# Kernel optimization log

Measured on AMD Instinct MI355X. Metric: run time of the kernel, lower is better.

## Reference

```python
import jax, jax.numpy as jnp
import numpy as np

N_NODES = 100000
N_EDGES = 1600000
N_GRAPHS = 1000
NODES_PER_GRAPH = 100  # batch vector is arange(N)//100: exactly 100 nodes per graph
HID = 32
MAX_Z = 1000
K = 30
D_LAT = HID * 3 + 1  # 97, total_latent_dim


def setup_inputs() -> dict:
    key = jax.random.key(0)
    ks = jax.random.split(key, 24)
    s = 1.0 / np.sqrt(HID)
    inp = {
        "z": jax.random.randint(ks[0], (N_NODES,), 0, MAX_Z, dtype=jnp.int32),
        "edge_index": jax.random.randint(ks[1], (2, N_EDGES), 0, N_NODES, dtype=jnp.int32),
        "batch": (jnp.arange(N_NODES, dtype=jnp.int32) // NODES_PER_GRAPH),
        "edge_weight": jax.random.uniform(ks[2], (N_EDGES,), jnp.float32, 0.1, 1.0),
        "z_emb": jax.random.normal(ks[3], (MAX_Z, HID), jnp.float32) * 0.1,
        # GCNConv stack: [32->32, 32->32, 32->32, 32->1]
        "Wg1": jax.random.normal(ks[4], (HID, HID)) * s,
        "bg1": jnp.zeros((HID,), jnp.float32),
        "Wg2": jax.random.normal(ks[5], (HID, HID)) * s,
        "bg2": jnp.zeros((HID,), jnp.float32),
        "Wg3": jax.random.normal(ks[6], (HID, HID)) * s,
        "bg3": jnp.zeros((HID,), jnp.float32),
        "Wg4": jax.random.normal(ks[7], (HID, 1)) * s,
        "bg4": jnp.zeros((1,), jnp.float32),
        # Conv1d(1, 16, kernel=97, stride=97)
        "Wc1": jax.random.normal(ks[8], (16, D_LAT)) * (1.0 / np.sqrt(D_LAT)),
        "bc1": jnp.zeros((16,), jnp.float32),
        # Conv1d(16, 32, kernel=5, stride=1)
        "Wc2": jax.random.normal(ks[9], (32, 16, 5)) * (1.0 / np.sqrt(16 * 5)),
        "bc2": jnp.zeros((32,), jnp.float32),
        # Linear(352, 128), Linear(128, 1)
        "Wl1": jax.random.normal(ks[10], (352, 128)) * (1.0 / np.sqrt(352)),
        "bl1": jnp.zeros((128,), jnp.float32),
        "Wl2": jax.random.normal(ks[11], (128, 1)) * (1.0 / np.sqrt(128)),
        "bl2": jnp.zeros((1,), jnp.float32),
    }
    return inp


def gcn_conv(x, src, dst, ew, W, b, n):
    # PyG GCNConv: xW, add self-loops (weight 1), sym-normalize, aggregate at dst, + bias
    xw = x @ W
    deg = jax.ops.segment_sum(ew, dst, num_segments=n) + 1.0  # +1 for self loop
    dinv = jnp.where(deg > 0, jax.lax.rsqrt(deg), 0.0)
    norm = dinv[src] * ew * dinv[dst]                          # [E]
    out = jax.ops.segment_sum(norm[:, None] * xw[src], dst, num_segments=n)
    out = out + xw * (dinv * dinv)[:, None]                    # self-loop term
    return out + b


def _forward(z, edge_index, batch, edge_weight, z_emb, Wg1, bg1, Wg2, bg2, Wg3, bg3,
             Wg4, bg4, Wc1, bc1, Wc2, bc2, Wl1, bl1, Wl2, bl2):
    src, dst = edge_index[0], edge_index[1]
    n = z.shape[0]
    x = z_emb[z]                                              # [N, 32]
    xs = []
    h = x
    for W, b in ((Wg1, bg1), (Wg2, bg2), (Wg3, bg3), (Wg4, bg4)):
        h = jnp.tanh(gcn_conv(h, src, dst, edge_weight, W, b, n))
        xs.append(h)
    x = jnp.concatenate(xs, axis=-1)                          # [N, 97]
    # global_sort_pool: batch is uniform (100 nodes/graph) so dense batching is a reshape
    dense = x.reshape(N_GRAPHS, NODES_PER_GRAPH, D_LAT)       # [B, 100, 97]
    idx = jnp.argsort(-dense[:, :, -1], axis=1)[:, :K]        # sort desc by last channel
    top = jnp.take_along_axis(dense, idx[:, :, None], axis=1)  # [B, 30, 97]
    # Conv1d(1,16,97,stride=97) on flattened [B,1,30*97] == per-slot dense layer
    y = jax.nn.relu(jnp.einsum('bkd,cd->bck', top, Wc1) + bc1[None, :, None])  # [B,16,30]
    y = y.reshape(N_GRAPHS, 16, K // 2, 2).max(axis=-1)        # MaxPool1d(2,2) -> [B,16,15]
    y = jax.lax.conv_general_dilated(y, Wc2, (1,), 'VALID',
                                     dimension_numbers=('NCH', 'OIH', 'NCH'))
    y = jax.nn.relu(y + bc2[None, :, None])                    # [B,32,11]
    y = y.reshape(N_GRAPHS, -1)                                # [B,352]
    y = jax.nn.relu(y @ Wl1 + bl1)                             # dropout: eval mode, identity
    return y @ Wl2 + bl2                                       # [B,1]


def reference(z, edge_index, batch, edge_weight, z_emb, Wg1, bg1, Wg2, bg2, Wg3, bg3,
              Wg4, bg4, Wc1, bc1, Wc2, bc2, Wl1, bl1, Wl2, bl2):
    return _forward(z, edge_index, batch, edge_weight, z_emb, Wg1, bg1, Wg2, bg2, Wg3,
                    bg3, Wg4, bg4, Wc1, bc1, Wc2, bc2, Wl1, bl1, Wl2, bl2)
```

## Files before the change

kernel.cpp:

```cpp
#include <hip/hip_runtime.h>

#define HID 32
#define DLAT 97
#define NPG 100
#define TOPK 30
#define BKT_NODES 256
#define MAXBKT 512
#define EPB 4096


__global__ void binA_kernel(const int* __restrict__ dst, int* __restrict__ bucket_cnt, int E) {
    __shared__ int hist[MAXBKT];
    for (int t = threadIdx.x; t < MAXBKT; t += blockDim.x) hist[t] = 0;
    __syncthreads();
    int base = blockIdx.x * EPB;
    int lim = min(E, base + EPB);
    for (int e = base + threadIdx.x; e < lim; e += blockDim.x)
        atomicAdd(&hist[dst[e] >> 8], 1);
    __syncthreads();
    for (int t = threadIdx.x; t < MAXBKT; t += blockDim.x) {
        int v = hist[t];
        if (v) atomicAdd(&bucket_cnt[t], v);
    }
}

__global__ __launch_bounds__(MAXBKT) void bscan_kernel(const int* __restrict__ bucket_cnt,
                                                       int* __restrict__ bucket_start,
                                                       int* __restrict__ cursor) {
    __shared__ int sh[MAXBKT];
    int t = threadIdx.x;
    int v = bucket_cnt[t];
    sh[t] = v;
    __syncthreads();
    for (int off = 1; off < MAXBKT; off <<= 1) {
        int tv = (t >= off) ? sh[t - off] : 0;
        __syncthreads();
        sh[t] += tv;
        __syncthreads();
    }
    int excl = sh[t] - v;
    bucket_start[t] = excl;
    cursor[t] = excl;
    if (t == MAXBKT - 1) bucket_start[MAXBKT] = sh[t];
}

__global__ void binB_kernel(const int* __restrict__ src, const int* __restrict__ dst,
                            const float* __restrict__ ew, int* __restrict__ cursor,
                            int2* __restrict__ bedge, int E) {
    __shared__ int hist[MAXBKT];
    __shared__ int lcur[MAXBKT];
    for (int t = threadIdx.x; t < MAXBKT; t += blockDim.x) hist[t] = 0;
    __syncthreads();
    int base = blockIdx.x * EPB;
    int lim = min(E, base + EPB);
    for (int e = base + threadIdx.x; e < lim; e += blockDim.x)
        atomicAdd(&hist[dst[e] >> 8], 1);
    __syncthreads();
    for (int t = threadIdx.x; t < MAXBKT; t += blockDim.x) {
        int v = hist[t];
        lcur[t] = v ? atomicAdd(&cursor[t], v) : 0;
    }
    __syncthreads();
    for (int e = base + threadIdx.x; e < lim; e += blockDim.x) {
        int d = dst[e];
        int slot = atomicAdd(&lcur[d >> 8], 1);
        bedge[slot] = make_int2(src[e] | ((d & 255) << 20), __float_as_int(ew[e]));
    }
}

__global__ __launch_bounds__(BKT_NODES) void sortlocal_kernel(
    const int2* __restrict__ bedge, const int* __restrict__ bucket_start,
    int2* __restrict__ csr, int* __restrict__ row_start, float* __restrict__ dinv,
    int N, int E) {
    __shared__ int cnt[BKT_NODES];
    __shared__ float facc[BKT_NODES];
    __shared__ int sh[BKT_NODES];
    __shared__ int lcur[BKT_NODES];
    int b = blockIdx.x;
    int beg = bucket_start[b], end = bucket_start[b + 1];
    int t = threadIdx.x;
    cnt[t] = 0;
    facc[t] = 0.f;
    __syncthreads();
    for (int i = beg + t; i < end; i += BKT_NODES) {
        int2 e = bedge[i];
        int loc = e.x >> 20;
        atomicAdd(&cnt[loc], 1);
        atomicAdd(&facc[loc], __int_as_float(e.y));
    }
    __syncthreads();
    int n = b * BKT_NODES + t;
    if (n < N) dinv[n] = 1.0f / sqrtf(1.0f + facc[t]);
    int v = cnt[t];
    sh[t] = v;
    __syncthreads();
    for (int off = 1; off < BKT_NODES; off <<= 1) {
        int tv = (t >= off) ? sh[t - off] : 0;
        __syncthreads();
        sh[t] += tv;
        __syncthreads();
    }
    int excl = sh[t] - v;
    lcur[t] = excl;
    if (n < N) row_start[n] = beg + excl;
    if (b == 0 && t == 0) row_start[N] = E;
    __syncthreads();
    for (int i = beg + t; i < end; i += BKT_NODES) {
        int2 e = bedge[i];
        int slot = atomicAdd(&lcur[e.x >> 20], 1);
        csr[beg + slot] = make_int2(e.x & 0xFFFFF, e.y);
    }
}

__global__ void xw1_kernel(const int* __restrict__ z, const float* __restrict__ z_emb,
                           const float* __restrict__ W, const float* __restrict__ dinv,
                           float* __restrict__ xw, int N) {
    int tid = blockIdx.x * blockDim.x + threadIdx.x;
    if (tid >= N * HID) return;
    int n = tid >> 5, f = tid & 31;
    const float* row = z_emb + (size_t)z[n] * HID;
    float s = 0.f;
#pragma unroll
    for (int k = 0; k < HID; ++k) s += row[k] * W[k * HID + f];
    xw[tid] = s * dinv[n];
}

template <int MODE>
__global__ __launch_bounds__(256) void agg32f_kernel(
    const int* __restrict__ row_start, const int2* __restrict__ csr,
    const float* __restrict__ xw, const float* __restrict__ b,
    const float* __restrict__ dinv, const float* __restrict__ Wn,
    float* __restrict__ concat, int col_off, float* __restrict__ xw_next, int N) {
    int tid = blockIdx.x * blockDim.x + threadIdx.x;
    int n = tid >> 5;
    if (n >= N) return;
    int f = threadIdx.x & 31;
    int beg = row_start[n], end = row_start[n + 1];
    float s0 = 0.f, s1 = 0.f;
    for (int i = beg; i < end; i += 8) {
        float w[8];
        int idx[8];
#pragma unroll
        for (int j = 0; j < 8; ++j) {
            int ii = min(i + j, end - 1);
            int2 v = csr[ii];
            idx[j] = v.x;
            w[j] = (i + j < end) ? __int_as_float(v.y) : 0.f;
        }
        float x[8];
#pragma unroll
        for (int j = 0; j < 8; ++j) x[j] = xw[(size_t)idx[j] * HID + f];
#pragma unroll
        for (int j = 0; j < 8; ++j) {
            if (j & 1) s1 += w[j] * x[j];
            else       s0 += w[j] * x[j];
        }
    }
    float s = s0 + s1;
    float di = dinv[n];
    float outv = tanhf(di * (s + xw[(size_t)n * HID + f]) + b[f]);
    concat[(size_t)n * DLAT + col_off + f] = outv;

    if (MODE == 0) {
        float p = 0.f;
#pragma unroll
        for (int k = 0; k < HID; ++k) {
            float ok = __shfl(outv, k, 32);
            p += ok * Wn[k * HID + f];
        }
        xw_next[(size_t)n * HID + f] = p * di;
    } else {
        float p = outv * Wn[f];
        p += __shfl_xor(p, 16);
        p += __shfl_xor(p, 8);
        p += __shfl_xor(p, 4);
        p += __shfl_xor(p, 2);
        p += __shfl_xor(p, 1);
        if (f == 0) xw_next[n] = p * di;
    }
}

__global__ __launch_bounds__(128) void topk_head_kernel(
    const int* __restrict__ row_start, const int2* __restrict__ csr,
    const float* __restrict__ xw4, const float* __restrict__ b4,
    const float* __restrict__ dinv, const float* __restrict__ concat,
    const float* __restrict__ Wc1, const float* __restrict__ bc1,
    const float* __restrict__ Wc2, const float* __restrict__ bc2,
    const float* __restrict__ Wl1, const float* __restrict__ bl1,
    const float* __restrict__ Wl2, const float* __restrict__ bl2,
    float* __restrict__ out) {
    int g = blockIdx.x;
    int tid = threadIdx.x;
    __shared__ float v[NPG];
    __shared__ int tidx[TOPK];
    __shared__ float tval[TOPK];
    __shared__ float top[TOPK * DLAT];
    __shared__ float y1[16 * TOPK];
    __shared__ float y2[16 * 15];
    __shared__ float y3[352];
    __shared__ float r[128];

    if (tid < NPG) {
        int n = g * NPG + tid;
        int beg = row_start[n], end = row_start[n + 1];
        float s = 0.f;
        for (int i = beg; i < end; ++i) {
            int2 e = csr[i];
            s += __int_as_float(e.y) * xw4[e.x];
        }
        v[tid] = tanhf(dinv[n] * (s + xw4[n]) + b4[0]);
    }
    __syncthreads();
    if (tid < NPG) {
        float vi = v[tid];
        int cnt = 0;
#pragma unroll 4
        for (int j = 0; j < NPG; ++j) {
            float vj = v[j];
            cnt += (vj > vi) || (vj == vi && j < tid);
        }
        if (cnt < TOPK) {
            tidx[cnt] = g * NPG + tid;
            tval[cnt] = vi;
        }
    }
    __syncthreads();

    for (int idx = tid; idx < TOPK * DLAT; idx += 128) {
        int k = idx / DLAT, d = idx - k * DLAT;
        top[idx] = (d == 96) ? tval[k] : concat[(size_t)tidx[k] * DLAT + d];
    }
    __syncthreads();

    for (int idx = tid; idx < 16 * TOPK; idx += 128) {
        int c = idx / TOPK, k = idx % TOPK;
        float s = bc1[c];
        const float* w = Wc1 + c * DLAT;
        const float* t = top + k * DLAT;
#pragma unroll 4
        for (int d = 0; d < DLAT; ++d) s += t[d] * w[d];
        y1[c * TOPK + k] = fmaxf(s, 0.f);
    }
    __syncthreads();

    for (int idx = tid; idx < 16 * 15; idx += 128) {
        int c = idx / 15, j = idx % 15;
        y2[idx] = fmaxf(y1[c * TOPK + 2 * j], y1[c * TOPK + 2 * j + 1]);
    }
    __syncthreads();

    for (int idx = tid; idx < 352; idx += 128) {
        int o = idx / 11, t = idx % 11;
        float s = bc2[o];
#pragma unroll
        for (int i = 0; i < 16; ++i) {
#pragma unroll
            for (int k = 0; k < 5; ++k)
                s += Wc2[(o * 16 + i) * 5 + k] * y2[i * 15 + t + k];
        }
        y3[idx] = fmaxf(s, 0.f);
    }
    __syncthreads();

    {
        float s = bl1[tid];
        for (int d = 0; d < 352; ++d) s += y3[d] * Wl1[d * 128 + tid];
        r[tid] = fmaxf(s, 0.f) * Wl2[tid];
    }
    __syncthreads();
    if (tid < 64) r[tid] += r[tid + 64];
    __syncthreads();
    if (tid == 0) {
        float s = 0.f;
        for (int j = 0; j < 64; ++j) s += r[j];
        out[g] = s + bl2[0];
    }
}


extern "C" void kernel_launch(void* const* d_in, const int* in_sizes, int n_in,
                              void* d_out, int out_size, void* d_ws, size_t ws_size,
                              hipStream_t stream) {
    const int* z = (const int*)d_in[0];
    const int* ei = (const int*)d_in[1];
    const float* ew = (const float*)d_in[3];
    const float* z_emb = (const float*)d_in[4];
    const float* Wg[4] = {(const float*)d_in[5], (const float*)d_in[7],
                          (const float*)d_in[9], (const float*)d_in[11]};
    const float* bg[4] = {(const float*)d_in[6], (const float*)d_in[8],
                          (const float*)d_in[10], (const float*)d_in[12]};
    const float* Wc1 = (const float*)d_in[13];
    const float* bc1 = (const float*)d_in[14];
    const float* Wc2 = (const float*)d_in[15];
    const float* bc2 = (const float*)d_in[16];
    const float* Wl1 = (const float*)d_in[17];
    const float* bl1 = (const float*)d_in[18];
    const float* Wl2 = (const float*)d_in[19];
    const float* bl2 = (const float*)d_in[20];
    float* out = (float*)d_out;

    const int N = in_sizes[0];
    const int E = in_sizes[1] / 2;
    const int G = out_size;
    const int* src = ei;
    const int* dst = ei + E;

    auto cdiv = [](long long a, long long b) { return (int)((a + b - 1) / b); };
    const int NB = cdiv(E, EPB);
    const int NBKT = cdiv(N, BKT_NODES);

    char* ws = (char*)d_ws;
    int2* bedge = (int2*)ws;                  ws += sizeof(int2) * (size_t)E;
    int2* csr = (int2*)ws;                    ws += sizeof(int2) * (size_t)E;
    int* bucket_cnt = (int*)ws;               ws += sizeof(int) * MAXBKT;
    int* bucket_start = (int*)ws;             ws += sizeof(int) * (MAXBKT + 1);
    int* cursor = (int*)ws;                   ws += sizeof(int) * MAXBKT;
    int* row_start = (int*)ws;                ws += sizeof(int) * (N + 1);
    float* dinv = (float*)ws;                 ws += sizeof(float) * N;
    float* xw_a = (float*)ws;                 ws += sizeof(float) * (size_t)N * HID;
    float* concat = (float*)ws;               ws += sizeof(float) * (size_t)N * DLAT;
    float* xw4 = (float*)ws;                  ws += sizeof(float) * N;
    float* xw_b = (float*)bedge;

    const int B = 256;

    hipMemsetAsync(bucket_cnt, 0, sizeof(int) * MAXBKT, stream);
    binA_kernel<<<NB, B, 0, stream>>>(dst, bucket_cnt, E);
    bscan_kernel<<<1, MAXBKT, 0, stream>>>(bucket_cnt, bucket_start, cursor);
    binB_kernel<<<NB, B, 0, stream>>>(src, dst, ew, cursor, bedge, E);
    sortlocal_kernel<<<NBKT, BKT_NODES, 0, stream>>>(bedge, bucket_start, csr, row_start,
                                                     dinv, N, E);

    xw1_kernel<<<cdiv((long long)N * HID, B), B, 0, stream>>>(z, z_emb, Wg[0], dinv, xw_a, N);
    const int AGGB = cdiv((long long)N * 32, B);
    agg32f_kernel<0><<<AGGB, B, 0, stream>>>(row_start, csr, xw_a, bg[0], dinv, Wg[1],
                                             concat, 0, xw_b, N);
    agg32f_kernel<0><<<AGGB, B, 0, stream>>>(row_start, csr, xw_b, bg[1], dinv, Wg[2],
                                             concat, 32, xw_a, N);
    agg32f_kernel<1><<<AGGB, B, 0, stream>>>(row_start, csr, xw_a, bg[2], dinv, Wg[3],
                                             concat, 64, xw4, N);

    topk_head_kernel<<<G, 128, 0, stream>>>(row_start, csr, xw4, bg[3], dinv, concat,
                                            Wc1, bc1, Wc2, bc2, Wl1, bl1, Wl2, bl2, out);
}
```

Before: 423.1 us.

## Stage bucket edges in LDS and shrink buckets for CSR build

```diff
diff --git a/kernel.cpp b/kernel.cpp
--- a/kernel.cpp
+++ b/kernel.cpp
@@ -4,21 +4,24 @@
 #define DLAT 97
 #define NPG 100
 #define TOPK 30
-#define BKT_NODES 256
-#define MAXBKT 512
-#define EPB 4096
-
-
-__global__ void binA_kernel(const int* __restrict__ dst, int* __restrict__ bucket_cnt, int E) {
+#define BKT_NODES 128
+#define BKT_SHIFT 7
+#define MAXBKT 1024
+#define CAP 3072
+#define CHUNK 8192
+
+
+__global__ __launch_bounds__(256) void binA_kernel(const int* __restrict__ dst,
+                                                   int* __restrict__ bucket_cnt, int E) {
     __shared__ int hist[MAXBKT];
-    for (int t = threadIdx.x; t < MAXBKT; t += blockDim.x) hist[t] = 0;
-    __syncthreads();
-    int base = blockIdx.x * EPB;
-    int lim = min(E, base + EPB);
-    for (int e = base + threadIdx.x; e < lim; e += blockDim.x)
-        atomicAdd(&hist[dst[e] >> 8], 1);
-    __syncthreads();
-    for (int t = threadIdx.x; t < MAXBKT; t += blockDim.x) {
+    for (int t = threadIdx.x; t < MAXBKT; t += 256) hist[t] = 0;
+    __syncthreads();
+    int base = blockIdx.x * CHUNK;
+    int lim = min(E, base + CHUNK);
+    for (int e = base + threadIdx.x; e < lim; e += 256)
+        atomicAdd(&hist[dst[e] >> BKT_SHIFT], 1);
+    __syncthreads();
+    for (int t = threadIdx.x; t < MAXBKT; t += 256) {
         int v = hist[t];
         if (v) atomicAdd(&bucket_cnt[t], v);
     }
@@ -44,71 +47,119 @@
     if (t == MAXBKT - 1) bucket_start[MAXBKT] = sh[t];
 }
 
-__global__ void binB_kernel(const int* __restrict__ src, const int* __restrict__ dst,
-                            const float* __restrict__ ew, int* __restrict__ cursor,
-                            int2* __restrict__ bedge, int E) {
+__global__ __launch_bounds__(256) void binB_kernel(const int* __restrict__ src,
+                                                   const int* __restrict__ dst,
+                                                   const float* __restrict__ ew,
+                                                   int* __restrict__ cursor,
+                                                   int2* __restrict__ bedge, int E) {
     __shared__ int hist[MAXBKT];
     __shared__ int lcur[MAXBKT];
-    for (int t = threadIdx.x; t < MAXBKT; t += blockDim.x) hist[t] = 0;
-    __syncthreads();
-    int base = blockIdx.x * EPB;
-    int lim = min(E, base + EPB);
-    for (int e = base + threadIdx.x; e < lim; e += blockDim.x)
-        atomicAdd(&hist[dst[e] >> 8], 1);
-    __syncthreads();
-    for (int t = threadIdx.x; t < MAXBKT; t += blockDim.x) {
+    __shared__ int dcache[CHUNK];
+    for (int t = threadIdx.x; t < MAXBKT; t += 256) hist[t] = 0;
+    __syncthreads();
+    int base = blockIdx.x * CHUNK;
+    int M = min(E - base, CHUNK);
+    for (int i = threadIdx.x; i < M; i += 256) {
+        int d = dst[base + i];
+        dcache[i] = d;
+        atomicAdd(&hist[d >> BKT_SHIFT], 1);
+    }
+    __syncthreads();
+    for (int t = threadIdx.x; t < MAXBKT; t += 256) {
         int v = hist[t];
         lcur[t] = v ? atomicAdd(&cursor[t], v) : 0;
     }
     __syncthreads();
-    for (int e = base + threadIdx.x; e < lim; e += blockDim.x) {
-        int d = dst[e];
-        int slot = atomicAdd(&lcur[d >> 8], 1);
-        bedge[slot] = make_int2(src[e] | ((d & 255) << 20), __float_as_int(ew[e]));
-    }
-}
-
-__global__ __launch_bounds__(BKT_NODES) void sortlocal_kernel(
+    for (int i = threadIdx.x; i < M; i += 256) {
+        int d = dcache[i];
+        int slot = atomicAdd(&lcur[d >> BKT_SHIFT], 1);
+        bedge[slot] = make_int2(src[base + i] | ((d & (BKT_NODES - 1)) << 20),
+                                __float_as_int(ew[base + i]));
+    }
+}
+
+__global__ __launch_bounds__(256) void sortlocal_kernel(
     const int2* __restrict__ bedge, const int* __restrict__ bucket_start,
     int2* __restrict__ csr, int* __restrict__ row_start, float* __restrict__ dinv,
     int N, int E) {
+    __shared__ int2 LDSe[CAP];
     __shared__ int cnt[BKT_NODES];
-    __shared__ float facc[BKT_NODES];
     __shared__ int sh[BKT_NODES];
     __shared__ int lcur[BKT_NODES];
-    int b = blockIdx.x;
-    int beg = bucket_start[b], end = bucket_start[b + 1];
-    int t = threadIdx.x;
-    cnt[t] = 0;
-    facc[t] = 0.f;
-    __syncthreads();
-    for (int i = beg + t; i < end; i += BKT_NODES) {
-        int2 e = bedge[i];
-        int loc = e.x >> 20;
-        atomicAdd(&cnt[loc], 1);
-        atomicAdd(&facc[loc], __int_as_float(e.y));
-    }
+    __shared__ float facc[BKT_NODES];
+    int b = blockIdx.x, t = threadIdx.x;
+    int beg = bucket_start[b], end = bucket_start[b + 1], M = end - beg;
+    if (t < BKT_NODES) { cnt[t] = 0; facc[t] = 0.f; }
     __syncthreads();
     int n = b * BKT_NODES + t;
-    if (n < N) dinv[n] = 1.0f / sqrtf(1.0f + facc[t]);
-    int v = cnt[t];
-    sh[t] = v;
-    __syncthreads();
-    for (int off = 1; off < BKT_NODES; off <<= 1) {
-        int tv = (t >= off) ? sh[t - off] : 0;
-        __syncthreads();
-        sh[t] += tv;
-        __syncthreads();
-    }
-    int excl = sh[t] - v;
-    lcur[t] = excl;
-    if (n < N) row_start[n] = beg + excl;
-    if (b == 0 && t == 0) row_start[N] = E;
-    __syncthreads();
-    for (int i = beg + t; i < end; i += BKT_NODES) {
-        int2 e = bedge[i];
-        int slot = atomicAdd(&lcur[e.x >> 20], 1);
-        csr[beg + slot] = make_int2(e.x & 0xFFFFF, e.y);
+    if (M <= CAP) {
+        for (int i = t; i < M; i += 256) {
+            int2 e = bedge[beg + i];
+            LDSe[i] = e;
+            atomicAdd(&cnt[(e.x >> 20) & (BKT_NODES - 1)], 1);
+        }
+        __syncthreads();
+        int v = 0;
+        if (t < BKT_NODES) { v = cnt[t]; sh[t] = v; }
+        __syncthreads();
+        for (int off = 1; off < BKT_NODES; off <<= 1) {
+            int tv = (t >= off && t < BKT_NODES) ? sh[t - off] : 0;
+            __syncthreads();
+            if (t < BKT_NODES) sh[t] += tv;
+            __syncthreads();
+        }
+        int excl = 0;
+        if (t < BKT_NODES) {
+            excl = sh[t] - v;
+            lcur[t] = excl;
+            if (n < N) row_start[n] = beg + excl;
+        }
+        if (b == 0 && t == 0) row_start[N] = E;
+        __syncthreads();
+        for (int i = t; i < M; i += 256) {
+            int2 e = LDSe[i];
+            int slot = atomicAdd(&lcur[(e.x >> 20) & (BKT_NODES - 1)], 1);
+            csr[beg + slot] = make_int2(e.x & 0xFFFFF, e.y);
+        }
+        __syncthreads();
+        if (t < BKT_NODES && n < N) {
+            float s = 1.f;
+            int s0 = beg + excl;
+            for (int i = 0; i < v; ++i) s += __int_as_float(csr[s0 + i].y);
+            dinv[n] = 1.f / sqrtf(s);
+        }
+    } else {
+        for (int i = beg + t; i < end; i += 256) {
+            int2 e = bedge[i];
+            int loc = (e.x >> 20) & (BKT_NODES - 1);
+            atomicAdd(&cnt[loc], 1);
+            atomicAdd(&facc[loc], __int_as_float(e.y));
+        }
+        __syncthreads();
+        int v = 0;
+        if (t < BKT_NODES) { v = cnt[t]; sh[t] = v; }
+        __syncthreads();
+        for (int off = 1; off < BKT_NODES; off <<= 1) {
+            int tv = (t >= off && t < BKT_NODES) ? sh[t - off] : 0;
+            __syncthreads();
+            if (t < BKT_NODES) sh[t] += tv;
+            __syncthreads();
+        }
+        if (t < BKT_NODES) {
+            int excl = sh[t] - v;
+            lcur[t] = excl;
+            if (n < N) {
+                row_start[n] = beg + excl;
+                dinv[n] = 1.f / sqrtf(1.f + facc[t]);
+            }
+        }
+        if (b == 0 && t == 0) row_start[N] = E;
+        __syncthreads();
+        for (int i = beg + t; i < end; i += 256) {
+            int2 e = bedge[i];
+            int slot = atomicAdd(&lcur[(e.x >> 20) & (BKT_NODES - 1)], 1);
+            csr[beg + slot] = make_int2(e.x & 0xFFFFF, e.y);
+        }
     }
 }
 
@@ -306,7 +357,7 @@
     const int* dst = ei + E;
 
     auto cdiv = [](long long a, long long b) { return (int)((a + b - 1) / b); };
-    const int NB = cdiv(E, EPB);
+    const int NB = cdiv(E, CHUNK);
     const int NBKT = cdiv(N, BKT_NODES);
 
     char* ws = (char*)d_ws;
@@ -328,8 +379,8 @@
     binA_kernel<<<NB, B, 0, stream>>>(dst, bucket_cnt, E);
     bscan_kernel<<<1, MAXBKT, 0, stream>>>(bucket_cnt, bucket_start, cursor);
     binB_kernel<<<NB, B, 0, stream>>>(src, dst, ew, cursor, bedge, E);
-    sortlocal_kernel<<<NBKT, BKT_NODES, 0, stream>>>(bedge, bucket_start, csr, row_start,
-                                                     dinv, N, E);
+    sortlocal_kernel<<<NBKT, B, 0, stream>>>(bedge, bucket_start, csr, row_start,
+                                             dinv, N, E);
 
     xw1_kernel<<<cdiv((long long)N * HID, B), B, 0, stream>>>(z, z_emb, Wg[0], dinv, xw_a, N);
     const int AGGB = cdiv((long long)N * 32, B);
```

Result: no change. 417.5 us (-1.3%).
